# Kernel tuning notes

Measured on AMD Instinct MI355X. Metric: run time of the kernel, lower is better.

## Reference

```python
import jax, jax.numpy as jnp
import numpy as np

N_NODES = 50000
N_EDGES = 1600000
IN_CH = 256
LAT = 32
HID = 64
OUT_CH = 256
GAT_H = 32  # GAT hidden dims [32, 32], heads=1


def setup_inputs() -> dict:
    key = jax.random.key(0)
    ks = jax.random.split(key, 30)
    nrm = lambda k, shape, s=0.05: jax.random.normal(k, shape, dtype=jnp.float32) * s
    inp = {}
    inp["x"] = jax.random.normal(ks[0], (N_NODES, IN_CH), dtype=jnp.float32)
    inp["edge_index"] = jax.random.randint(ks[1], (2, N_EDGES), 0, N_NODES)
    # GAT layer 1: IN_CH -> 32 (heads=1), layer 2: 32 -> 32, final linear 32 -> LAT
    inp["W_g1"] = nrm(ks[2], (IN_CH, GAT_H)); inp["as_g1"] = nrm(ks[3], (GAT_H,)); inp["ad_g1"] = nrm(ks[4], (GAT_H,)); inp["b_g1"] = jnp.zeros((GAT_H,), jnp.float32)
    inp["W_g2"] = nrm(ks[5], (GAT_H, GAT_H)); inp["as_g2"] = nrm(ks[6], (GAT_H,)); inp["ad_g2"] = nrm(ks[7], (GAT_H,)); inp["b_g2"] = jnp.zeros((GAT_H,), jnp.float32)
    inp["W_gf"] = nrm(ks[8], (GAT_H, LAT)); inp["b_gf"] = jnp.zeros((LAT,), jnp.float32)
    inp["W_m1"] = nrm(ks[9], (IN_CH, HID)); inp["b_m1"] = jnp.zeros((HID,), jnp.float32); inp["g_m1"] = jnp.ones((HID,), jnp.float32); inp["be_m1"] = jnp.zeros((HID,), jnp.float32)
    inp["W_m2"] = nrm(ks[10], (HID, HID)); inp["b_m2"] = jnp.zeros((HID,), jnp.float32); inp["g_m2"] = jnp.ones((HID,), jnp.float32); inp["be_m2"] = jnp.zeros((HID,), jnp.float32)
    inp["W_m3"] = nrm(ks[11], (HID, LAT)); inp["b_m3"] = jnp.zeros((LAT,), jnp.float32); inp["g_m3"] = jnp.ones((LAT,), jnp.float32); inp["be_m3"] = jnp.zeros((LAT,), jnp.float32)
    # final linear LAT -> OUT_CH + ReLU
    inp["W_f"] = nrm(ks[12], (LAT, OUT_CH)); inp["b_f"] = jnp.zeros((OUT_CH,), jnp.float32)
    return inp


def _bn_relu(h, g, b):
    # BatchNorm1d in training mode: batch stats, biased variance, eps=1e-5
    m = jnp.mean(h, axis=0)
    v = jnp.var(h, axis=0)
    return jax.nn.relu((h - m) * jax.lax.rsqrt(v + 1e-5) * g + b)


def _gat(h_in, src, dst, W, a_s, a_d, b):
    # PyG GATConv (heads=1): edge (src j -> dst i), e = LeakyReLU(a_src.Wx_j + a_dst.Wx_i)
    N = h_in.shape[0]
    h = h_in @ W                                   # [N, F]
    e = jax.nn.leaky_relu((h @ a_s)[src] + (h @ a_d)[dst], 0.2)  # [E]
    m = jax.ops.segment_max(e, dst, num_segments=N)              # scatter-softmax over incoming edges
    ex = jnp.exp(e - m[dst])
    den = jax.ops.segment_sum(ex, dst, num_segments=N)
    alpha = ex / den[dst]
    out = jax.ops.segment_sum(alpha[:, None] * h[src], dst, num_segments=N)
    return out + b


def reference(x, edge_index, W_g1, as_g1, ad_g1, b_g1, W_g2, as_g2, ad_g2, b_g2, W_gf, b_gf, W_m1, b_m1, g_m1, be_m1, W_m2, b_m2, g_m2, be_m2, W_m3, b_m3, g_m3, be_m3, W_f, b_f):
    N = x.shape[0]
    loops = jnp.arange(N)
    src = jnp.concatenate([edge_index[0], loops])  # PyG add_self_loops=True
    dst = jnp.concatenate([edge_index[1], loops])
    r = _bn_relu(x @ W_m1 + b_m1, g_m1, be_m1)
    r = _bn_relu(r @ W_m2 + b_m2, g_m2, be_m2)
    r = _bn_relu(r @ W_m3 + b_m3, g_m3, be_m3)
    # GAT interpolation branch (dropout inactive in eval)
    h = jax.nn.relu(_gat(x, src, dst, W_g1, as_g1, ad_g1, b_g1))
    h = jax.nn.relu(_gat(h, src, dst, W_g2, as_g2, ad_g2, b_g2))
    h = h @ W_gf + b_gf
    # blend with alphas = 0.5 constant vector
    out = 0.5 * r + 0.5 * h
    return jax.nn.relu(out @ W_f + b_f)
```

## Files before the change

kernel.cpp:

```cpp
#include <hip/hip_runtime.h>

#define NNODES 50000
#define NEDGES 1600000
#define NBUCK 196
#define BIN_CH 4096
#define CNT_CH 4096

__device__ __forceinline__ float leaky02(float x) { return x > 0.f ? x : 0.2f * x; }

__device__ __forceinline__ int block_incl_scan(int v, int* sh) {
  int t = threadIdx.x;
  sh[t] = v;
  __syncthreads();
  for (int d = 1; d < 256; d <<= 1) {
    int u = (t >= d) ? sh[t - d] : 0;
    __syncthreads();
    sh[t] += u;
    __syncthreads();
  }
  return sh[t];
}

__global__ __launch_bounds__(256) void k_b0(const int* __restrict__ dst,
                                            int* __restrict__ gcnt, int E) {
  __shared__ int hist[256];
  int t = threadIdx.x;
  hist[t] = 0;
  __syncthreads();
  int base0 = blockIdx.x * CNT_CH;
#pragma unroll
  for (int r = 0; r < CNT_CH / 256; ++r) {
    int idx = base0 + r * 256 + t;
    if (idx < E) atomicAdd(&hist[dst[idx] >> 8], 1);
  }
  __syncthreads();
  if (t < NBUCK && hist[t]) atomicAdd(&gcnt[t], hist[t]);
}

__global__ __launch_bounds__(256) void k_b1(const int* __restrict__ gcnt,
                                            int* __restrict__ base,
                                            int* __restrict__ cursor) {
  __shared__ int sh[256];
  int t = threadIdx.x;
  int v = (t < NBUCK) ? gcnt[t] : 0;
  int incl = block_incl_scan(v, sh);
  if (t < NBUCK) {
    base[t] = incl - v;
    cursor[t] = incl - v;
  }
  if (t == 255) base[NBUCK] = NEDGES;
}

__global__ __launch_bounds__(256) void k_bin(const int* __restrict__ src,
                                             const int* __restrict__ dst,
                                             int* __restrict__ cursor,
                                             unsigned* __restrict__ binned, int E) {
  __shared__ int hist[256];
  __shared__ int cur[256];
  int t = threadIdx.x;
  int base0 = blockIdx.x * BIN_CH;
  unsigned pk[BIN_CH / 256];
  hist[t] = 0;
  __syncthreads();
#pragma unroll
  for (int r = 0; r < BIN_CH / 256; ++r) {
    int idx = base0 + r * 256 + t;
    if (idx < E) {
      unsigned p = ((unsigned)dst[idx] << 16) | (unsigned)src[idx];
      pk[r] = p;
      atomicAdd(&hist[p >> 24], 1);
    }
  }
  __syncthreads();
  if (t < NBUCK && hist[t]) cur[t] = atomicAdd(&cursor[t], hist[t]);
  __syncthreads();
#pragma unroll
  for (int r = 0; r < BIN_CH / 256; ++r) {
    int idx = base0 + r * 256 + t;
    if (idx < E) {
      unsigned p = pk[r];
      int pos = atomicAdd(&cur[p >> 24], 1);
      binned[pos] = p;
    }
  }
}

__global__ __launch_bounds__(256) void k_sort(const unsigned* __restrict__ binned,
                                              const int* __restrict__ base,
                                              int* __restrict__ deg,
                                              int* __restrict__ offs,
                                              int* __restrict__ csr) {
  __shared__ int hist[256];
  __shared__ int scanbuf[256];
  __shared__ int cur[256];
  int t = threadIdx.x;
  int b = blockIdx.x;
  int lo = base[b], hi = base[b + 1];
  int node0 = b << 8;
  hist[t] = 0;
  __syncthreads();
  for (int i = lo + t; i < hi; i += 256)
    atomicAdd(&hist[(binned[i] >> 16) & 255], 1);
  __syncthreads();
  int h = hist[t];
  int incl = block_incl_scan(h, scanbuf);
  int excl = incl - h;
  int node = node0 + t;
  if (node < NNODES) {
    deg[node] = h;
    offs[node] = lo + excl;
  }
  cur[t] = lo + excl;
  __syncthreads();
  for (int i = lo + t; i < hi; i += 256) {
    unsigned p = binned[i];
    int pos = atomicAdd(&cur[(p >> 16) & 255], 1);
    csr[pos] = (int)(p & 0xFFFFu);
  }
}

template <int K, int NC, int TN, int SPLIT, bool BN, bool STATS, int ROWS>
__global__ __launch_bounds__(256) void k_gemm(
    const float* __restrict__ A, const float* __restrict__ bn_sum,
    const float* __restrict__ bn_sq, const float* __restrict__ bn_gamma,
    const float* __restrict__ bn_beta, float invM,
    const float* __restrict__ B0, const float* __restrict__ B1,
    const float* __restrict__ bias0,
    float* __restrict__ out0, float* __restrict__ out1,
    float* __restrict__ gsum, float* __restrict__ gsq, int M) {
  constexpr int KC = 64;
  constexpr int RPT = ROWS / 16;
  __shared__ float As[ROWS * KC];
  __shared__ float Bs[KC * NC];
  __shared__ float scS[BN ? K : 4];
  __shared__ float shS[BN ? K : 4];
  const int tid = threadIdx.x;
  const int row0 = blockIdx.x * ROWS;
  const int cg = tid & 15;
  const int rowg = (tid >> 4) & 15;
  const int swz = (rowg & 3) << 2;

  if constexpr (BN) {
    if (tid < K) {
      float mean = bn_sum[tid] * invM;
      float var = bn_sq[tid] * invM - mean * mean;
      float rs = rsqrtf(var + 1e-5f);
      float sc = rs * bn_gamma[tid];
      scS[tid] = sc;
      shS[tid] = bn_beta[tid] - mean * sc;
    }
    __syncthreads();
  }

  float acc[RPT][TN];
#pragma unroll
  for (int r = 0; r < RPT; ++r)
#pragma unroll
    for (int j = 0; j < TN; ++j) acc[r][j] = 0.f;

  constexpr int KB = KC / 4;
  for (int k0 = 0; k0 < K; k0 += KC) {
#pragma unroll
    for (int it = 0; it < (ROWS * KB) / 256; ++it) {
      int idx = tid + it * 256;
      int row = idx / KB;
      int kb = idx % KB;
      float4 v = make_float4(0.f, 0.f, 0.f, 0.f);
      int grow = row0 + row;
      if (grow < M) {
        v = *reinterpret_cast<const float4*>(&A[(size_t)grow * K + k0 + kb * 4]);
        if constexpr (BN) {
          int kb4 = k0 + kb * 4;
          float4 sc = *reinterpret_cast<const float4*>(&scS[kb4]);
          float4 sf = *reinterpret_cast<const float4*>(&shS[kb4]);
          v.x = fmaxf(v.x * sc.x + sf.x, 0.f);
          v.y = fmaxf(v.y * sc.y + sf.y, 0.f);
          v.z = fmaxf(v.z * sc.z + sf.z, 0.f);
          v.w = fmaxf(v.w * sc.w + sf.w, 0.f);
        }
      }
      *reinterpret_cast<float4*>(&As[row * KC + ((kb ^ (row & 3)) * 4)]) = v;
    }
    {
      constexpr int KB0 = SPLIT / 4;
#pragma unroll
      for (int it = 0; it < (KC * KB0) / 256; ++it) {
        int idx = tid + it * 256;
        int kk = idx / KB0;
        int cb = idx % KB0;
        float4 v = *reinterpret_cast<const float4*>(&B0[(size_t)(k0 + kk) * SPLIT + cb * 4]);
        *reinterpret_cast<float4*>(&Bs[kk * NC + cb * 4]) = v;
      }
    }
    if constexpr (NC > SPLIT) {
      constexpr int W1 = NC - SPLIT;
      constexpr int KB1 = W1 / 4;
#pragma unroll
      for (int it = 0; it < (KC * KB1) / 256; ++it) {
        int idx = tid + it * 256;
        int kk = idx / KB1;
        int cb = idx % KB1;
        float4 v = *reinterpret_cast<const float4*>(&B1[(size_t)(k0 + kk) * W1 + cb * 4]);
        *reinterpret_cast<float4*>(&Bs[kk * NC + SPLIT + cb * 4]) = v;
      }
    }
    __syncthreads();
    for (int kk = 0; kk < KC; kk += 4) {
      float4 a[RPT];
#pragma unroll
      for (int r = 0; r < RPT; ++r)
        a[r] = *reinterpret_cast<const float4*>(&As[(rowg + 16 * r) * KC + (kk ^ swz)]);
      float b[4][TN];
#pragma unroll
      for (int i = 0; i < 4; ++i)
#pragma unroll
        for (int j = 0; j < TN; ++j) b[i][j] = Bs[(kk + i) * NC + cg * TN + j];
#pragma unroll
      for (int r = 0; r < RPT; ++r)
#pragma unroll
        for (int j = 0; j < TN; ++j) {
          acc[r][j] += a[r].x * b[0][j];
          acc[r][j] += a[r].y * b[1][j];
          acc[r][j] += a[r].z * b[2][j];
          acc[r][j] += a[r].w * b[3][j];
        }
    }
    __syncthreads();
  }
  float bias_r[TN];
#pragma unroll
  for (int j = 0; j < TN; ++j) {
    int c = cg * TN + j;
    bias_r[j] = (c < SPLIT) ? bias0[c] : 0.f;
  }
  float cs[TN], cq[TN];
#pragma unroll
  for (int j = 0; j < TN; ++j) { cs[j] = 0.f; cq[j] = 0.f; }
#pragma unroll
  for (int r = 0; r < RPT; ++r) {
    int grow = row0 + rowg + 16 * r;
    if (grow < M) {
#pragma unroll
      for (int j = 0; j < TN; ++j) {
        int c = cg * TN + j;
        if (c < SPLIT) {
          float v = acc[r][j] + bias_r[j];
          out0[(size_t)grow * SPLIT + c] = v;
          if (STATS) { cs[j] += v; cq[j] += v * v; }
        } else {
          out1[(size_t)grow * (NC - SPLIT) + (c - SPLIT)] = acc[r][j];
        }
      }
    }
  }
  if constexpr (STATS) {
#pragma unroll
    for (int j = 0; j < TN; ++j) {
      cs[j] += __shfl_xor(cs[j], 16);
      cs[j] += __shfl_xor(cs[j], 32);
      cq[j] += __shfl_xor(cq[j], 16);
      cq[j] += __shfl_xor(cq[j], 32);
    }
    float* red = Bs;
    int wave = tid >> 6;
    int lane = tid & 63;
    if (lane < 16) {
#pragma unroll
      for (int j = 0; j < TN; ++j) {
        int c = cg * TN + j;
        if (c < SPLIT) {
          red[wave * 2 * SPLIT + c] = cs[j];
          red[wave * 2 * SPLIT + SPLIT + c] = cq[j];
        }
      }
    }
    __syncthreads();
    if (tid < SPLIT) {
      float s = red[tid] + red[2 * SPLIT + tid] + red[4 * SPLIT + tid] + red[6 * SPLIT + tid];
      atomicAdd(&gsum[tid], s);
    } else if (tid < 2 * SPLIT) {
      int c = tid - SPLIT;
      float q = red[SPLIT + c] + red[3 * SPLIT + c] + red[5 * SPLIT + c] + red[7 * SPLIT + c];
      atomicAdd(&gsq[c], q);
    }
  }
}

__global__ __launch_bounds__(256) void k_sdot(const float* __restrict__ g,
                                              const float* __restrict__ as_,
                                              const float* __restrict__ ad_,
                                              float* __restrict__ sv,
                                              float* __restrict__ dv, int N) {
  int lane = threadIdx.x & 31;
  int row = blockIdx.x * 8 + (threadIdx.x >> 5);
  if (row >= N) return;
  float v = g[(size_t)row * 32 + lane];
  float a = v * as_[lane];
  float b = v * ad_[lane];
#pragma unroll
  for (int w = 16; w >= 1; w >>= 1) {
    a += __shfl_xor(a, w);
    b += __shfl_xor(b, w);
  }
  if (lane == 0) {
    sv[row] = a;
    dv[row] = b;
  }
}

__global__ __launch_bounds__(256) void k_gat_agg(
    const float* __restrict__ h, const float* __restrict__ sv,
    const float* __restrict__ dv, const int* __restrict__ offs,
    const int* __restrict__ deg, const int* __restrict__ csr,
    const float* __restrict__ bias, float* __restrict__ out, int N) {
  int lane = threadIdx.x & 31;
  int node = blockIdx.x * 8 + (threadIdx.x >> 5);
  if (node >= N) return;
  int start = offs[node];
  int cnt = deg[node];
  float di = dv[node];
  float ex0 = __expf(leaky02(sv[node] + di));
  float den = ex0;
  float acc = ex0 * h[(size_t)node * 32 + lane];
  int k = 0;
  for (; k + 8 <= cnt; k += 8) {
    int j0 = csr[start + k + 0], j1 = csr[start + k + 1];
    int j2 = csr[start + k + 2], j3 = csr[start + k + 3];
    int j4 = csr[start + k + 4], j5 = csr[start + k + 5];
    int j6 = csr[start + k + 6], j7 = csr[start + k + 7];
    float s0 = sv[j0], s1 = sv[j1], s2 = sv[j2], s3 = sv[j3];
    float s4 = sv[j4], s5 = sv[j5], s6 = sv[j6], s7 = sv[j7];
    float h0 = h[(size_t)j0 * 32 + lane], h1 = h[(size_t)j1 * 32 + lane];
    float h2 = h[(size_t)j2 * 32 + lane], h3 = h[(size_t)j3 * 32 + lane];
    float h4 = h[(size_t)j4 * 32 + lane], h5 = h[(size_t)j5 * 32 + lane];
    float h6 = h[(size_t)j6 * 32 + lane], h7 = h[(size_t)j7 * 32 + lane];
    float e0 = __expf(leaky02(s0 + di)), e1 = __expf(leaky02(s1 + di));
    float e2 = __expf(leaky02(s2 + di)), e3 = __expf(leaky02(s3 + di));
    float e4 = __expf(leaky02(s4 + di)), e5 = __expf(leaky02(s5 + di));
    float e6 = __expf(leaky02(s6 + di)), e7 = __expf(leaky02(s7 + di));
    den += ((e0 + e1) + (e2 + e3)) + ((e4 + e5) + (e6 + e7));
    acc += e0 * h0 + e1 * h1 + e2 * h2 + e3 * h3;
    acc += e4 * h4 + e5 * h5 + e6 * h6 + e7 * h7;
  }
  for (; k < cnt; ++k) {
    int j = csr[start + k];
    float ex = __expf(leaky02(sv[j] + di));
    den += ex;
    acc += ex * h[(size_t)j * 32 + lane];
  }
  out[(size_t)node * 32 + lane] = fmaxf(acc / den + bias[lane], 0.f);
}

__global__ __launch_bounds__(256) void k_small_gemm_sd(
    const float* __restrict__ hin, const float* __restrict__ W,
    const float* __restrict__ as_, const float* __restrict__ ad_,
    float* __restrict__ gout, float* __restrict__ sv, float* __restrict__ dv,
    int N) {
  __shared__ float Ws[32][32];
  {
    int t = threadIdx.x;
#pragma unroll
    for (int r = 0; r < 4; ++r) {
      int idx = t + r * 256;
      Ws[idx >> 5][idx & 31] = W[idx];
    }
  }
  __syncthreads();
  int lane = threadIdx.x & 31;
  int row = blockIdx.x * 8 + (threadIdx.x >> 5);
  if (row >= N) return;
  float hv = hin[(size_t)row * 32 + lane];
  float acc = 0.f;
#pragma unroll
  for (int k = 0; k < 32; ++k) acc += __shfl(hv, k, 32) * Ws[k][lane];
  gout[(size_t)row * 32 + lane] = acc;
  float a = acc * as_[lane];
  float b = acc * ad_[lane];
#pragma unroll
  for (int w = 16; w >= 1; w >>= 1) {
    a += __shfl_xor(a, w);
    b += __shfl_xor(b, w);
  }
  if (lane == 0) {
    sv[row] = a;
    dv[row] = b;
  }
}

__global__ __launch_bounds__(256) void k_final2(
    const float* __restrict__ mlp3, const float* __restrict__ sum3,
    const float* __restrict__ sq3, const float* __restrict__ g3,
    const float* __restrict__ be3, float invM, const float* __restrict__ h2,
    const float* __restrict__ Wgf, const float* __restrict__ bgf,
    const float* __restrict__ Wf, const float* __restrict__ bf,
    float* __restrict__ out, int N) {
  __shared__ float WfS[32 * 256];
  __shared__ float Bl[64][36];
  __shared__ float WgfS[32][33];
  __shared__ float colS[3][32];
  const int t = threadIdx.x;
  const int row0 = blockIdx.x * 64;

  {
    const float4* src = reinterpret_cast<const float4*>(Wf);
    float4* dst = reinterpret_cast<float4*>(WfS);
#pragma unroll
    for (int r = 0; r < 8; ++r) dst[t + r * 256] = src[t + r * 256];
  }
#pragma unroll
  for (int r = 0; r < 4; ++r) {
    int idx = t + r * 256;
    WgfS[idx >> 5][idx & 31] = Wgf[idx];
  }
  if (t < 32) {
    float mean = sum3[t] * invM;
    float var = sq3[t] * invM - mean * mean;
    float rs = rsqrtf(var + 1e-5f);
    float sc = rs * g3[t];
    colS[0][t] = sc;
    colS[1][t] = be3[t] - mean * sc;
    colS[2][t] = bgf[t];
  }
#pragma unroll
  for (int r = 0; r < 2; ++r) {
    int idx = t + r * 256;
    int row = idx >> 3;
    int k4 = idx & 7;
    int grow = row0 + row;
    float4 v = make_float4(0.f, 0.f, 0.f, 0.f);
    if (grow < N) v = *reinterpret_cast<const float4*>(&h2[(size_t)grow * 32 + k4 * 4]);
    *reinterpret_cast<float4*>(&Bl[row][k4 * 4]) = v;
  }
  __syncthreads();

  const int col = t & 31;
  const int rb = t >> 5;
  float w[32];
#pragma unroll
  for (int k = 0; k < 32; ++k) w[k] = WgfS[k][col];
  float bl[8];
#pragma unroll
  for (int r = 0; r < 8; ++r) {
    int row = rb + 8 * r;
    float a = colS[2][col];
#pragma unroll
    for (int k4 = 0; k4 < 8; ++k4) {
      float4 hv = *reinterpret_cast<const float4*>(&Bl[row][k4 * 4]);
      a += hv.x * w[k4 * 4 + 0] + hv.y * w[k4 * 4 + 1] +
           hv.z * w[k4 * 4 + 2] + hv.w * w[k4 * 4 + 3];
    }
    int grow = row0 + row;
    float pre = (grow < N) ? mlp3[(size_t)grow * 32 + col] : 0.f;
    float rv = fmaxf(pre * colS[0][col] + colS[1][col], 0.f);
    bl[r] = 0.5f * rv + 0.5f * a;
  }
  __syncthreads();
#pragma unroll
  for (int r = 0; r < 8; ++r) Bl[rb + 8 * r][col] = bl[r];
  __syncthreads();

  const int cg = t & 31;
  const int rowg = t >> 5;
  const float4* Wf4 = reinterpret_cast<const float4*>(WfS);
  float4 acc0[8], acc1[8];
#pragma unroll
  for (int r = 0; r < 8; ++r) {
    acc0[r] = make_float4(0.f, 0.f, 0.f, 0.f);
    acc1[r] = make_float4(0.f, 0.f, 0.f, 0.f);
  }
  for (int k = 0; k < 32; k += 4) {
    float4 a[8];
#pragma unroll
    for (int r = 0; r < 8; ++r)
      a[r] = *reinterpret_cast<const float4*>(&Bl[rowg + 8 * r][k]);
    float4 b0[4], b1[4];
#pragma unroll
    for (int i = 0; i < 4; ++i) {
      b0[i] = Wf4[(k + i) * 64 + cg];
      b1[i] = Wf4[(k + i) * 64 + cg + 32];
    }
#pragma unroll
    for (int r = 0; r < 8; ++r) {
      float av[4] = {a[r].x, a[r].y, a[r].z, a[r].w};
#pragma unroll
      for (int i = 0; i < 4; ++i) {
        acc0[r].x += av[i] * b0[i].x;
        acc0[r].y += av[i] * b0[i].y;
        acc0[r].z += av[i] * b0[i].z;
        acc0[r].w += av[i] * b0[i].w;
        acc1[r].x += av[i] * b1[i].x;
        acc1[r].y += av[i] * b1[i].y;
        acc1[r].z += av[i] * b1[i].z;
        acc1[r].w += av[i] * b1[i].w;
      }
    }
  }
  float4 bfA = reinterpret_cast<const float4*>(bf)[cg];
  float4 bfB = reinterpret_cast<const float4*>(bf)[cg + 32];
  float4* out4 = reinterpret_cast<float4*>(out);
#pragma unroll
  for (int r = 0; r < 8; ++r) {
    int grow = row0 + rowg + 8 * r;
    if (grow < N) {
      float4 o0 = acc0[r], o1 = acc1[r];
      o0.x = fmaxf(o0.x + bfA.x, 0.f); o0.y = fmaxf(o0.y + bfA.y, 0.f);
      o0.z = fmaxf(o0.z + bfA.z, 0.f); o0.w = fmaxf(o0.w + bfA.w, 0.f);
      o1.x = fmaxf(o1.x + bfB.x, 0.f); o1.y = fmaxf(o1.y + bfB.y, 0.f);
      o1.z = fmaxf(o1.z + bfB.z, 0.f); o1.w = fmaxf(o1.w + bfB.w, 0.f);
      out4[(size_t)grow * 64 + cg] = o0;
      out4[(size_t)grow * 64 + cg + 32] = o1;
    }
  }
}

extern "C" void kernel_launch(void* const* d_in, const int* in_sizes, int n_in,
                              void* d_out, int out_size, void* d_ws, size_t ws_size,
                              hipStream_t stream) {
  const float* x = (const float*)d_in[0];
  const int* edge = (const int*)d_in[1];
  const float* W_g1 = (const float*)d_in[2];
  const float* as_g1 = (const float*)d_in[3];
  const float* ad_g1 = (const float*)d_in[4];
  const float* b_g1 = (const float*)d_in[5];
  const float* W_g2 = (const float*)d_in[6];
  const float* as_g2 = (const float*)d_in[7];
  const float* ad_g2 = (const float*)d_in[8];
  const float* b_g2 = (const float*)d_in[9];
  const float* W_gf = (const float*)d_in[10];
  const float* b_gf = (const float*)d_in[11];
  const float* W_m1 = (const float*)d_in[12];
  const float* b_m1 = (const float*)d_in[13];
  const float* g_m1 = (const float*)d_in[14];
  const float* be_m1 = (const float*)d_in[15];
  const float* W_m2 = (const float*)d_in[16];
  const float* b_m2 = (const float*)d_in[17];
  const float* g_m2 = (const float*)d_in[18];
  const float* be_m2 = (const float*)d_in[19];
  const float* W_m3 = (const float*)d_in[20];
  const float* b_m3 = (const float*)d_in[21];
  const float* g_m3 = (const float*)d_in[22];
  const float* be_m3 = (const float*)d_in[23];
  const float* W_f = (const float*)d_in[24];
  const float* b_f = (const float*)d_in[25];
  float* out = (float*)d_out;

  const int N = NNODES, E = NEDGES;
  const float invM = 1.f / N;
  const int* esrc = edge;
  const int* edst = edge + E;

  float* ws = (float*)d_ws;
  float* g1 = ws;
  float* mlp1 = g1 + (size_t)N * 32;
  float* mlp2 = mlp1 + (size_t)N * 64;
  float* mlp3 = mlp2 + (size_t)N * 64;
  float* h1 = mlp3 + (size_t)N * 32;
  float* g2 = h1 + (size_t)N * 32;
  float* h2 = g2 + (size_t)N * 32;
  float* s1 = h2 + (size_t)N * 32;
  float* d1 = s1 + N;
  float* s2 = d1 + N;
  float* d2 = s2 + N;
  float* stats = d2 + N;
  float* sum1 = stats, *sq1 = stats + 64;
  float* sum2 = stats + 128, *sq2 = stats + 192;
  float* sum3 = stats + 256, *sq3 = stats + 288;
  int* ip = (int*)(stats + 384);
  int* gcnt = ip;
  int* base = gcnt + 256;
  int* cursor = base + 256;
  int* deg = cursor + 256;
  int* offs = deg + N;
  int* csr = offs + N;
  unsigned* binned = (unsigned*)mlp2;

  hipMemsetAsync(gcnt, 0, 256 * sizeof(int), stream);
  hipMemsetAsync(stats, 0, 384 * sizeof(float), stream);

  k_b0<<<(E + CNT_CH - 1) / CNT_CH, 256, 0, stream>>>(edst, gcnt, E);
  k_b1<<<1, 256, 0, stream>>>(gcnt, base, cursor);
  k_bin<<<(E + BIN_CH - 1) / BIN_CH, 256, 0, stream>>>(esrc, edst, cursor, binned, E);
  k_sort<<<NBUCK, 256, 0, stream>>>(binned, base, deg, offs, csr);

  const int GB64 = (N + 63) / 64;
  const int GB128 = (N + 127) / 128;

  k_gemm<256, 96, 6, 64, false, true, 64><<<GB64, 256, 0, stream>>>(
      x, nullptr, nullptr, nullptr, nullptr, invM, W_m1, W_g1, b_m1,
      mlp1, g1, sum1, sq1, N);
  k_sdot<<<(N + 7) / 8, 256, 0, stream>>>(g1, as_g1, ad_g1, s1, d1, N);
  k_gat_agg<<<(N + 7) / 8, 256, 0, stream>>>(g1, s1, d1, offs, deg, csr, b_g1, h1, N);

  k_gemm<64, 64, 4, 64, true, true, 128><<<GB128, 256, 0, stream>>>(
      mlp1, sum1, sq1, g_m1, be_m1, invM, W_m2, nullptr, b_m2,
      mlp2, nullptr, sum2, sq2, N);

  k_small_gemm_sd<<<(N + 7) / 8, 256, 0, stream>>>(h1, W_g2, as_g2, ad_g2, g2, s2, d2, N);
  k_gat_agg<<<(N + 7) / 8, 256, 0, stream>>>(g2, s2, d2, offs, deg, csr, b_g2, h2, N);

  k_gemm<64, 32, 2, 32, true, true, 128><<<GB128, 256, 0, stream>>>(
      mlp2, sum2, sq2, g_m2, be_m2, invM, W_m3, nullptr, b_m3,
      mlp3, nullptr, sum3, sq3, N);

  k_final2<<<(N + 63) / 64, 256, 0, stream>>>(mlp3, sum3, sq3, g_m3, be_m3, invM,
                                              h2, W_gf, b_gf, W_f, b_f, out, N);
}
```

Measured before the change: 413.8 us.

## Replace first fused GEMM with split-bf16 MFMA kernel emulating fp32 precision

Replaces the scalar-FMA first-layer GEMM (x times [W_m1|W_g1], K=256, 96 outputs) with a kernel using bf16 MFMA 16x16x32 instructions. Each fp32 operand is split into bf16 hi and lo parts and three MFMAs per tile (hi*hi, lo*hi, hi*lo) approximate fp32 accuracy. A small pre-kernel splits and transposes the weights into a scratch region. A register double-buffered load loop and the fused bias and BN-statistics epilogue are kept. This trades extra MFMA work and a reduction in precision for matrix-core throughput on a GEMM that reads the full 51 MB input.

Measured after the change: 420.2 us. No clear change (+1.6%).

```diff
diff --git a/kernel.cpp b/kernel.cpp
--- a/kernel.cpp
+++ b/kernel.cpp
@@ -5,6 +5,9 @@
 #define NBUCK 196
 #define BIN_CH 4096
 #define CNT_CH 4096
+
+typedef __attribute__((ext_vector_type(4))) float f32x4;
+typedef __attribute__((ext_vector_type(8))) short short8;
 
 __device__ __forceinline__ float leaky02(float x) { return x > 0.f ? x : 0.2f * x; }
 
@@ -283,6 +286,159 @@
       float q = red[SPLIT + c] + red[3 * SPLIT + c] + red[5 * SPLIT + c] + red[7 * SPLIT + c];
       atomicAdd(&gsq[c], q);
     }
+  }
+}
+
+__global__ __launch_bounds__(256) void k_bsplit(const float* __restrict__ Wm,
+                                                const float* __restrict__ Wg,
+                                                unsigned short* __restrict__ Bth,
+                                                unsigned short* __restrict__ Btl) {
+  int col = blockIdx.x;
+  int k = threadIdx.x;
+  float v = (col < 64) ? Wm[k * 64 + col] : Wg[k * 32 + (col - 64)];
+  unsigned b = __float_as_uint(v);
+  unsigned h = b & 0xffff0000u;
+  float lo = v - __uint_as_float(h);
+  Bth[col * 256 + k] = (unsigned short)(h >> 16);
+  Btl[col * 256 + k] = (unsigned short)(__float_as_uint(lo) >> 16);
+}
+
+union U16 { uint4 u; short8 s; };
+__device__ __forceinline__ short8 as_s8(uint4 u) { U16 t; t.u = u; return t.s; }
+
+__device__ __forceinline__ void split2(float x0, float x1, unsigned& h, unsigned& l) {
+  unsigned b0 = __float_as_uint(x0), b1 = __float_as_uint(x1);
+  unsigned h0 = b0 & 0xffff0000u, h1 = b1 & 0xffff0000u;
+  h = (h0 >> 16) | h1;
+  float l0 = x0 - __uint_as_float(h0);
+  float l1 = x1 - __uint_as_float(h1);
+  l = (__float_as_uint(l0) >> 16) | (__float_as_uint(l1) & 0xffff0000u);
+}
+
+__device__ __forceinline__ void split8(const float4& a, const float4& b,
+                                       short8& hi, short8& lo) {
+  uint4 h, l;
+  split2(a.x, a.y, h.x, l.x);
+  split2(a.z, a.w, h.y, l.y);
+  split2(b.x, b.y, h.z, l.z);
+  split2(b.z, b.w, h.w, l.w);
+  hi = as_s8(h);
+  lo = as_s8(l);
+}
+
+__global__ __launch_bounds__(256, 2) void k_gemm1_mfma(
+    const float* __restrict__ A, const unsigned short* __restrict__ Bth,
+    const unsigned short* __restrict__ Btl, const float* __restrict__ bias0,
+    float* __restrict__ out0, float* __restrict__ out1,
+    float* __restrict__ gsum, float* __restrict__ gsq, int M) {
+  __shared__ float red[512];
+  const int tid = threadIdx.x;
+  const int wv = tid >> 6;
+  const int lane = tid & 63;
+  const int lg = lane >> 4;
+  const int lc = lane & 15;
+  const int rowb = blockIdx.x * 128 + wv * 32;
+
+  const int r0 = rowb + lc;
+  const int r1 = rowb + 16 + lc;
+  const bool v0ok = r0 < M, v1ok = r1 < M;
+  const float* a0p = A + (size_t)r0 * 256 + lg * 8;
+  const float* a1p = A + (size_t)r1 * 256 + lg * 8;
+  const unsigned short* bhp = Bth + (size_t)lc * 256 + lg * 8;
+  const unsigned short* blp = Btl + (size_t)lc * 256 + lg * 8;
+  const float4 fz = make_float4(0.f, 0.f, 0.f, 0.f);
+
+  float4 araw[2][2][2];
+  uint4 bhr[2][6], blr[2][6];
+  f32x4 acc[2][6];
+#pragma unroll
+  for (int rf = 0; rf < 2; ++rf)
+#pragma unroll
+    for (int cf = 0; cf < 6; ++cf) acc[rf][cf] = (f32x4){0.f, 0.f, 0.f, 0.f};
+
+#pragma unroll
+  for (int c = 0; c < 9; ++c) {
+    if (c < 8) {
+      const int buf = c & 1;
+      const int off = c * 32;
+      araw[buf][0][0] = v0ok ? *reinterpret_cast<const float4*>(a0p + off) : fz;
+      araw[buf][0][1] = v0ok ? *reinterpret_cast<const float4*>(a0p + off + 4) : fz;
+      araw[buf][1][0] = v1ok ? *reinterpret_cast<const float4*>(a1p + off) : fz;
+      araw[buf][1][1] = v1ok ? *reinterpret_cast<const float4*>(a1p + off + 4) : fz;
+#pragma unroll
+      for (int cf = 0; cf < 6; ++cf) {
+        bhr[buf][cf] = *reinterpret_cast<const uint4*>(bhp + cf * 4096 + off);
+        blr[buf][cf] = *reinterpret_cast<const uint4*>(blp + cf * 4096 + off);
+      }
+    }
+    if (c > 0) {
+      const int buf = (c - 1) & 1;
+      short8 ah[2], al[2], bh[6], bl[6];
+#pragma unroll
+      for (int rf = 0; rf < 2; ++rf)
+        split8(araw[buf][rf][0], araw[buf][rf][1], ah[rf], al[rf]);
+#pragma unroll
+      for (int cf = 0; cf < 6; ++cf) {
+        bh[cf] = as_s8(bhr[buf][cf]);
+        bl[cf] = as_s8(blr[buf][cf]);
+      }
+#pragma unroll
+      for (int rf = 0; rf < 2; ++rf)
+#pragma unroll
+        for (int cf = 0; cf < 6; ++cf) {
+          acc[rf][cf] = __builtin_amdgcn_mfma_f32_16x16x32_bf16(ah[rf], bh[cf], acc[rf][cf], 0, 0, 0);
+          acc[rf][cf] = __builtin_amdgcn_mfma_f32_16x16x32_bf16(al[rf], bh[cf], acc[rf][cf], 0, 0, 0);
+          acc[rf][cf] = __builtin_amdgcn_mfma_f32_16x16x32_bf16(ah[rf], bl[cf], acc[rf][cf], 0, 0, 0);
+        }
+    }
+  }
+
+  float bias_r[4];
+#pragma unroll
+  for (int cf = 0; cf < 4; ++cf) bias_r[cf] = bias0[cf * 16 + lc];
+  float cs[4] = {0.f, 0.f, 0.f, 0.f}, cq[4] = {0.f, 0.f, 0.f, 0.f};
+#pragma unroll
+  for (int rf = 0; rf < 2; ++rf) {
+    int rbase = rowb + rf * 16 + lg * 4;
+#pragma unroll
+    for (int i = 0; i < 4; ++i) {
+      int row = rbase + i;
+      if (row < M) {
+#pragma unroll
+        for (int cf = 0; cf < 4; ++cf) {
+          float v = acc[rf][cf][i] + bias_r[cf];
+          out0[(size_t)row * 64 + cf * 16 + lc] = v;
+          cs[cf] += v;
+          cq[cf] += v * v;
+        }
+#pragma unroll
+        for (int cf = 4; cf < 6; ++cf)
+          out1[(size_t)row * 32 + (cf - 4) * 16 + lc] = acc[rf][cf][i];
+      }
+    }
+  }
+#pragma unroll
+  for (int cf = 0; cf < 4; ++cf) {
+    cs[cf] += __shfl_xor(cs[cf], 16);
+    cs[cf] += __shfl_xor(cs[cf], 32);
+    cq[cf] += __shfl_xor(cq[cf], 16);
+    cq[cf] += __shfl_xor(cq[cf], 32);
+  }
+  if (lg == 0) {
+#pragma unroll
+    for (int cf = 0; cf < 4; ++cf) {
+      red[wv * 128 + cf * 16 + lc] = cs[cf];
+      red[wv * 128 + 64 + cf * 16 + lc] = cq[cf];
+    }
+  }
+  __syncthreads();
+  if (tid < 64) {
+    float s = red[tid] + red[128 + tid] + red[256 + tid] + red[384 + tid];
+    atomicAdd(&gsum[tid], s);
+  } else if (tid < 128) {
+    int cc = tid - 64;
+    float q = red[64 + cc] + red[192 + cc] + red[320 + cc] + red[448 + cc];
+    atomicAdd(&gsq[cc], q);
   }
 }
 
@@ -573,21 +729,22 @@
   int* offs = deg + N;
   int* csr = offs + N;
   unsigned* binned = (unsigned*)mlp2;
+  unsigned short* Bth = (unsigned short*)((char*)mlp2 + (size_t)E * 4);
+  unsigned short* Btl = Bth + 96 * 256;
 
   hipMemsetAsync(gcnt, 0, 256 * sizeof(int), stream);
   hipMemsetAsync(stats, 0, 384 * sizeof(float), stream);
+
+  k_bsplit<<<96, 256, 0, stream>>>(W_m1, W_g1, Bth, Btl);
 
   k_b0<<<(E + CNT_CH - 1) / CNT_CH, 256, 0, stream>>>(edst, gcnt, E);
   k_b1<<<1, 256, 0, stream>>>(gcnt, base, cursor);
   k_bin<<<(E + BIN_CH - 1) / BIN_CH, 256, 0, stream>>>(esrc, edst, cursor, binned, E);
   k_sort<<<NBUCK, 256, 0, stream>>>(binned, base, deg, offs, csr);
 
-  const int GB64 = (N + 63) / 64;
   const int GB128 = (N + 127) / 128;
 
-  k_gemm<256, 96, 6, 64, false, true, 64><<<GB64, 256, 0, stream>>>(
-      x, nullptr, nullptr, nullptr, nullptr, invM, W_m1, W_g1, b_m1,
-      mlp1, g1, sum1, sq1, N);
+  k_gemm1_mfma<<<GB128, 256, 0, stream>>>(x, Bth, Btl, b_m1, mlp1, g1, sum1, sq1, N);
   k_sdot<<<(N + 7) / 8, 256, 0, stream>>>(g1, as_g1, ad_g1, s1, d1, N);
   k_gat_agg<<<(N + 7) / 8, 256, 0, stream>>>(g1, s1, d1, offs, deg, csr, b_g1, h1, N);
 
```
